# Kernel tuning notes

Measured on AMD Instinct MI355X. Metric: run time of the kernel, lower is better.

## Reference

```python
import jax, jax.numpy as jnp
import numpy as np

H = 8          # num_heads
DH = 16        # head dim = out_dim // num_heads
D = 128        # out_dim = in_dim
EPS_BN = 1e-5


def _batchnorm(h, gamma, beta):
    mu = h.mean(axis=0)
    var = h.var(axis=0)  # biased, matches torch BatchNorm1d training
    return (h - mu) / jnp.sqrt(var + EPS_BN) * gamma + beta


def setup_inputs() -> dict:
    key = jax.random.key(0)
    ks = jax.random.split(key, 16)
    N, E = 50000, 600000
    s = 1.0 / np.sqrt(D)
    inp = {
        "x": jax.random.normal(ks[0], (N, D), jnp.float32),
        "edge_attr": jax.random.normal(ks[1], (E, D), jnp.float32),
        "edge_index": jax.random.randint(ks[2], (2, E), 0, N, jnp.int64),
        # attention projections (no bias, use_bias=False)
        "Wq": jax.random.normal(ks[3], (D, D), jnp.float32) * s,
        "Wk": jax.random.normal(ks[4], (D, D), jnp.float32) * s,
        "We": jax.random.normal(ks[5], (D, D), jnp.float32) * s,
        "Wv": jax.random.normal(ks[6], (D, D), jnp.float32) * s,
        # batchnorm 1
        "bn1_g": jnp.ones((D,), jnp.float32),
        "bn1_b": jnp.zeros((D,), jnp.float32),
        # FFN
        "W1": jax.random.normal(ks[7], (D, 2 * D), jnp.float32) * s,
        "b1": jnp.zeros((2 * D,), jnp.float32),
        "W2": jax.random.normal(ks[8], (2 * D, D), jnp.float32) * (1.0 / np.sqrt(2 * D)),
        "b2": jnp.zeros((D,), jnp.float32),
        # batchnorm 2
        "bn2_g": jnp.ones((D,), jnp.float32),
        "bn2_b": jnp.zeros((D,), jnp.float32),
    }
    return inp


def _forward(x, edge_attr, edge_index, Wq, Wk, We, Wv, bn1_g, bn1_b,
             W1, b1, W2, b2, bn2_g, bn2_b):
    N = x.shape[0]
    src, dst = edge_index[0], edge_index[1]

    # projections -> [N, H, DH] / [E, H, DH]
    Q_h = (x @ Wq).reshape(N, H, DH)
    K_h = (x @ Wk).reshape(N, H, DH)
    V_h = (x @ Wv).reshape(N, H, DH)
    E_e = (edge_attr @ We).reshape(-1, H, DH)

    # edge-wise multiplicative attention score
    score = K_h[src] * Q_h[dst] / np.sqrt(DH) * E_e      # [E, H, DH]
    score = jnp.exp(jnp.clip(score.sum(-1, keepdims=True), -5.0, 5.0))  # [E, H, 1]

    msg = V_h[src] * score                               # [E, H, DH]
    wV = jax.ops.segment_sum(msg, dst, num_segments=N)   # [N, H, DH]
    Z = jax.ops.segment_sum(score, dst, num_segments=N)  # [N, H, 1]

    h_attn = (wV / (Z + 1e-6)).reshape(N, D)

    # residual + batchnorm (dropout=0)
    h = x + h_attn
    h = _batchnorm(h, bn1_g, bn1_b)

    # FFN with residual + batchnorm
    h2 = jax.nn.relu(h @ W1 + b1)
    h2 = h2 @ W2 + b2
    h = h + h2
    h = _batchnorm(h, bn2_g, bn2_b)
    return h


def reference(x, edge_attr, edge_index, Wq, Wk, We, Wv, bn1_g, bn1_b,
              W1, b1, W2, b2, bn2_g, bn2_b):
    return _forward(x, edge_attr, edge_index, Wq, Wk, We, Wv, bn1_g, bn1_b,
                    W1, b1, W2, b2, bn2_g, bn2_b)
```

## Files before the change

### kernel.cpp

```cpp
#include <hip/hip_runtime.h>
#include <hip/hip_bf16.h>
#include <math.h>
#include <stdint.h>

#define NN 50000
#define EE 600000

#define QH_OFF   0
#define K_OFF    6400000
#define V_OFF    12800000
#define HMID_OFF 6400000
#define HFIN_OFF 19200000
#define ROWS_OFF 19200000
#define CNT_OFF  19260000
#define CUR_OFF  19310000
#define ELS_OFF  19360000
#define ELE_OFF  19960000
#define ST_OFF   25600000
#define FLAG_OFF 25601024
#define H_OFF    QH_OFF

__global__ void detect_eidx(const int* __restrict__ e32, float* __restrict__ ws) {
  __shared__ int nz;
  if (threadIdx.x == 0) nz = 0;
  __syncthreads();
  if (e32[threadIdx.x * 2 + 1] != 0) atomicAdd(&nz, 1);
  __syncthreads();
  if (threadIdx.x == 0) ((int*)(ws + FLAG_OFF))[0] = (nz == 0) ? 1 : 0;
}

__device__ __forceinline__ int load_idx(const void* eidx, int is64, size_t off) {
  return is64 ? (int)((const long long*)eidx)[off] : ((const int*)eidx)[off];
}

__global__ __launch_bounds__(256)
void count_deg(const void* __restrict__ eidx, float* __restrict__ ws) {
  int e = blockIdx.x * 256 + threadIdx.x;
  if (e >= EE) return;
  int is64 = ((const int*)(ws + FLAG_OFF))[0];
  int dst = load_idx(eidx, is64, (size_t)EE + e);
  atomicAdd((int*)(ws + CNT_OFF) + dst, 1);
}

__global__ __launch_bounds__(1024)
void scan_deg(float* __restrict__ ws) {
  const int* cnt = (const int*)(ws + CNT_OFF);
  int* rows = (int*)(ws + ROWS_OFF);
  __shared__ int part[1024];
  const int t = threadIdx.x;
  const int base = t * 49;
  int s = 0;
  for (int i = 0; i < 49; ++i) {
    int idx = base + i;
    s += (idx < NN) ? cnt[idx] : 0;
  }
  part[t] = s;
  __syncthreads();
  for (int off = 1; off < 1024; off <<= 1) {
    int v = (t >= off) ? part[t - off] : 0;
    __syncthreads();
    part[t] += v;
    __syncthreads();
  }
  int run = (t == 0) ? 0 : part[t - 1];
  for (int i = 0; i < 49; ++i) {
    int idx = base + i;
    if (idx < NN) {
      rows[idx] = run;
      run += cnt[idx];
    }
  }
  if (t == 1023) rows[NN] = EE;
}

__global__ __launch_bounds__(256)
void fill_csr(const void* __restrict__ eidx, float* __restrict__ ws) {
  int e = blockIdx.x * 256 + threadIdx.x;
  if (e >= EE) return;
  int is64 = ((const int*)(ws + FLAG_OFF))[0];
  int src = load_idx(eidx, is64, (size_t)e);
  int dst = load_idx(eidx, is64, (size_t)EE + e);
  int p = atomicAdd((int*)(ws + CUR_OFF) + dst, 1);
  int j = ((const int*)(ws + ROWS_OFF))[dst] + p;
  ((int*)(ws + ELS_OFF))[j] = src;
  ((int*)(ws + ELE_OFF))[j] = e;
}

__global__ __launch_bounds__(256)
void proj_qkv(const float* __restrict__ x, const float* __restrict__ Wq,
              const float* __restrict__ Wk, const float* __restrict__ Wv,
              float* __restrict__ ws) {
  __shared__ float As[32][68];
  __shared__ float Bs[32][128];
  const int tid = threadIdx.x;
  const int tx = tid & 15, ty = tid >> 4;
  const int row0 = blockIdx.x * 64;
  const float* W = (blockIdx.y == 0) ? Wq : ((blockIdx.y == 1) ? Wk : Wv);
  float* out = ws + ((blockIdx.y == 0) ? QH_OFF : ((blockIdx.y == 1) ? K_OFF : V_OFF));

  float acc[4][8];
#pragma unroll
  for (int i = 0; i < 4; ++i)
#pragma unroll
    for (int j = 0; j < 8; ++j) acc[i][j] = 0.f;

  for (int k0 = 0; k0 < 128; k0 += 32) {
#pragma unroll
    for (int j = 0; j < 2; ++j) {
      int s = tid + 256 * j;
      int r = s >> 3, kg = (s & 7) << 2;
      int gr = row0 + r;
      float4 v = make_float4(0.f, 0.f, 0.f, 0.f);
      if (gr < NN) v = *(const float4*)&x[(size_t)gr * 128 + k0 + kg];
      As[kg + 0][r] = v.x; As[kg + 1][r] = v.y; As[kg + 2][r] = v.z; As[kg + 3][r] = v.w;
    }
#pragma unroll
    for (int j = 0; j < 4; ++j) {
      int s = tid + 256 * j;
      int kk = s >> 5, cg = (s & 31) << 2;
      *(float4*)&Bs[kk][cg] = *(const float4*)&W[(size_t)(k0 + kk) * 128 + cg];
    }
    __syncthreads();
#pragma unroll
    for (int k = 0; k < 32; ++k) {
      float4 a4 = *(float4*)&As[k][ty << 2];
      float4 b4a = *(float4*)&Bs[k][tx << 3];
      float4 b4b = *(float4*)&Bs[k][(tx << 3) + 4];
      float av[4] = {a4.x, a4.y, a4.z, a4.w};
      float bv[8] = {b4a.x, b4a.y, b4a.z, b4a.w, b4b.x, b4b.y, b4b.z, b4b.w};
#pragma unroll
      for (int i = 0; i < 4; ++i)
#pragma unroll
        for (int j = 0; j < 8; ++j) acc[i][j] = fmaf(av[i], bv[j], acc[i][j]);
    }
    __syncthreads();
  }
#pragma unroll
  for (int i = 0; i < 4; ++i) {
    int gr = row0 + (ty << 2) + i;
    if (gr < NN) {
      float4 o0 = make_float4(acc[i][0], acc[i][1], acc[i][2], acc[i][3]);
      float4 o1 = make_float4(acc[i][4], acc[i][5], acc[i][6], acc[i][7]);
      *(float4*)&out[(size_t)gr * 128 + (tx << 3)] = o0;
      *(float4*)&out[(size_t)gr * 128 + (tx << 3) + 4] = o1;
    }
  }
}

__global__ __launch_bounds__(256)
void edge_score(const float* __restrict__ edge_attr, const void* __restrict__ eidx,
                const float* __restrict__ We, float* __restrict__ ws,
                float* __restrict__ score) {
  __shared__ float As[32][68];
  __shared__ float Bs[32][128];
  __shared__ int s_src[64], s_dst[64];
  __shared__ int s_is64;
  const int tid = threadIdx.x;
  const int tx = tid & 15, ty = tid >> 4;
  const int e0 = blockIdx.x * 64;

  if (tid == 0) s_is64 = ((const int*)(ws + FLAG_OFF))[0];
  __syncthreads();
  if (tid < 128) {
    int lane = tid & 63;
    size_t off = (tid < 64) ? (size_t)(e0 + lane) : ((size_t)EE + e0 + lane);
    int idx = s_is64 ? (int)((const long long*)eidx)[off]
                     : ((const int*)eidx)[off];
    if (tid < 64) s_src[lane] = idx; else s_dst[lane] = idx;
  }

  float acc[4][8];
#pragma unroll
  for (int i = 0; i < 4; ++i)
#pragma unroll
    for (int j = 0; j < 8; ++j) acc[i][j] = 0.f;

  for (int k0 = 0; k0 < 128; k0 += 32) {
#pragma unroll
    for (int j = 0; j < 2; ++j) {
      int s = tid + 256 * j;
      int r = s >> 3, kg = (s & 7) << 2;
      float4 v = *(const float4*)&edge_attr[(size_t)(e0 + r) * 128 + k0 + kg];
      As[kg + 0][r] = v.x; As[kg + 1][r] = v.y; As[kg + 2][r] = v.z; As[kg + 3][r] = v.w;
    }
#pragma unroll
    for (int j = 0; j < 4; ++j) {
      int s = tid + 256 * j;
      int kk = s >> 5, cg = (s & 31) << 2;
      *(float4*)&Bs[kk][cg] = *(const float4*)&We[(size_t)(k0 + kk) * 128 + cg];
    }
    __syncthreads();
#pragma unroll
    for (int k = 0; k < 32; ++k) {
      float4 a4 = *(float4*)&As[k][ty << 2];
      float4 b4a = *(float4*)&Bs[k][tx << 3];
      float4 b4b = *(float4*)&Bs[k][(tx << 3) + 4];
      float av[4] = {a4.x, a4.y, a4.z, a4.w};
      float bv[8] = {b4a.x, b4a.y, b4a.z, b4a.w, b4b.x, b4b.y, b4b.z, b4b.w};
#pragma unroll
      for (int i = 0; i < 4; ++i)
#pragma unroll
        for (int j = 0; j < 8; ++j) acc[i][j] = fmaf(av[i], bv[j], acc[i][j]);
    }
    __syncthreads();
  }

  const float* Qm = ws + QH_OFF;
  const float* Km = ws + K_OFF;
  const int c0 = tx << 3;

#pragma unroll
  for (int i = 0; i < 4; ++i) {
    const int e = e0 + (ty << 2) + i;
    const int src = s_src[(ty << 2) + i];
    const int dst = s_dst[(ty << 2) + i];
    const float* Kp = Km + (size_t)src * 128 + c0;
    const float* Qp = Qm + (size_t)dst * 128 + c0;
    float4 ka = *(const float4*)Kp, kb = *(const float4*)(Kp + 4);
    float4 qa = *(const float4*)Qp, qb = *(const float4*)(Qp + 4);
    float p = acc[i][0] * ka.x * qa.x + acc[i][1] * ka.y * qa.y
            + acc[i][2] * ka.z * qa.z + acc[i][3] * ka.w * qa.w
            + acc[i][4] * kb.x * qb.x + acc[i][5] * kb.y * qb.y
            + acc[i][6] * kb.z * qb.z + acc[i][7] * kb.w * qb.w;
    p *= 0.25f;
    p += __shfl_xor(p, 1);
    float sc = __expf(fminf(fmaxf(p, -5.f), 5.f));
    if ((tx & 1) == 0) score[(size_t)e * 8 + (tx >> 1)] = sc;
  }
}

__global__ __launch_bounds__(256)
void aggregate(const float* __restrict__ x, const float* __restrict__ score,
               float* __restrict__ ws) {
  const int* rows = (const int*)(ws + ROWS_OFF);
  const int* els  = (const int*)(ws + ELS_OFF);
  const int* ele  = (const int*)(ws + ELE_OFF);
  const float* V  = ws + V_OFF;
  float* h = ws + H_OFF;
  float* st = ws + ST_OFF;
  const int tid = threadIdx.x;
  const int l = tid & 31;
  const int g = tid >> 5;
  const int c = l << 2;
  const int h8 = l >> 2;

  float s4[4] = {0.f, 0.f, 0.f, 0.f}, q4[4] = {0.f, 0.f, 0.f, 0.f};

  for (int d = blockIdx.x * 8 + g; d < NN; d += gridDim.x * 8) {
    const int j0 = rows[d], j1 = rows[d + 1];
    float a0 = 0.f, a1 = 0.f, a2 = 0.f, a3 = 0.f, z = 0.f;
    int e = 0, src = 0;
    if (j0 < j1) { e = ele[j0]; src = els[j0]; }
    for (int j = j0; j < j1; ++j) {
      int e2 = 0, src2 = 0;
      if (j + 1 < j1) { e2 = ele[j + 1]; src2 = els[j + 1]; }
      float sc = score[(size_t)e * 8 + h8];
      float4 v4 = *(const float4*)&V[(size_t)src * 128 + c];
      a0 = fmaf(v4.x, sc, a0); a1 = fmaf(v4.y, sc, a1);
      a2 = fmaf(v4.z, sc, a2); a3 = fmaf(v4.w, sc, a3);
      z += sc;
      e = e2; src = src2;
    }
    float zi = 1.f / (z + 1e-6f);
    float4 xv = *(const float4*)&x[(size_t)d * 128 + c];
    float4 hv;
    hv.x = xv.x + a0 * zi; hv.y = xv.y + a1 * zi;
    hv.z = xv.z + a2 * zi; hv.w = xv.w + a3 * zi;
    *(float4*)&h[(size_t)d * 128 + c] = hv;
    s4[0] += hv.x; s4[1] += hv.y; s4[2] += hv.z; s4[3] += hv.w;
    q4[0] += hv.x * hv.x; q4[1] += hv.y * hv.y;
    q4[2] += hv.z * hv.z; q4[3] += hv.w * hv.w;
  }

  __shared__ float red[8][32][8];
#pragma unroll
  for (int j = 0; j < 4; ++j) { red[g][l][j] = s4[j]; red[g][l][4 + j] = q4[j]; }
  __syncthreads();
  if (tid < 32) {
    float ss[4] = {0.f, 0.f, 0.f, 0.f}, qq[4] = {0.f, 0.f, 0.f, 0.f};
    for (int gg = 0; gg < 8; ++gg)
#pragma unroll
      for (int j = 0; j < 4; ++j) { ss[j] += red[gg][tid][j]; qq[j] += red[gg][tid][4 + j]; }
#pragma unroll
    for (int j = 0; j < 4; ++j) {
      atomicAdd(&st[(tid << 2) + j], ss[j]);
      atomicAdd(&st[128 + (tid << 2) + j], qq[j]);
    }
  }
}

__global__ void bn_finalize(const float* __restrict__ g, const float* __restrict__ beta,
                            float* __restrict__ ws, int sum_off, int out_off) {
  float* st = ws + ST_OFF;
  int c = threadIdx.x;
  float mu = st[sum_off + c] / (float)NN;
  float var = st[sum_off + 128 + c] / (float)NN - mu * mu;
  float istd = 1.f / sqrtf(var + 1e-5f);
  float a = g[c] * istd;
  st[out_off + c] = a;
  st[out_off + 128 + c] = beta[c] - mu * a;
}

__global__ __launch_bounds__(256)
void ffn1(const float* __restrict__ W1, const float* __restrict__ b1, float* __restrict__ ws) {
  __shared__ float As[32][68];
  __shared__ float Bs[32][128];
  const float* h = ws + H_OFF;
  const float* a1 = ws + ST_OFF + 512;
  const float* bb1 = ws + ST_OFF + 640;
  float* hmid = ws + HMID_OFF;
  const int tid = threadIdx.x;
  const int tx = tid & 15, ty = tid >> 4;
  const int row0 = blockIdx.x * 64;
  const int c0 = blockIdx.y * 128;

  float acc[4][8];
#pragma unroll
  for (int i = 0; i < 4; ++i)
#pragma unroll
    for (int j = 0; j < 8; ++j) acc[i][j] = 0.f;

  for (int k0 = 0; k0 < 128; k0 += 32) {
#pragma unroll
    for (int j = 0; j < 2; ++j) {
      int s = tid + 256 * j;
      int r = s >> 3, kg = (s & 7) << 2;
      int gr = row0 + r;
      float4 v = make_float4(0.f, 0.f, 0.f, 0.f);
      if (gr < NN) {
        v = *(const float4*)&h[(size_t)gr * 128 + k0 + kg];
        float4 aa = *(const float4*)&a1[k0 + kg];
        float4 bb = *(const float4*)&bb1[k0 + kg];
        v.x = v.x * aa.x + bb.x; v.y = v.y * aa.y + bb.y;
        v.z = v.z * aa.z + bb.z; v.w = v.w * aa.w + bb.w;
      }
      As[kg + 0][r] = v.x; As[kg + 1][r] = v.y; As[kg + 2][r] = v.z; As[kg + 3][r] = v.w;
    }
#pragma unroll
    for (int j = 0; j < 4; ++j) {
      int s = tid + 256 * j;
      int kk = s >> 5, cg = (s & 31) << 2;
      *(float4*)&Bs[kk][cg] = *(const float4*)&W1[(size_t)(k0 + kk) * 256 + c0 + cg];
    }
    __syncthreads();
#pragma unroll
    for (int k = 0; k < 32; ++k) {
      float4 a4 = *(float4*)&As[k][ty << 2];
      float4 b4a = *(float4*)&Bs[k][tx << 3];
      float4 b4b = *(float4*)&Bs[k][(tx << 3) + 4];
      float av[4] = {a4.x, a4.y, a4.z, a4.w};
      float bv[8] = {b4a.x, b4a.y, b4a.z, b4a.w, b4b.x, b4b.y, b4b.z, b4b.w};
#pragma unroll
      for (int i = 0; i < 4; ++i)
#pragma unroll
        for (int j = 0; j < 8; ++j) acc[i][j] = fmaf(av[i], bv[j], acc[i][j]);
    }
    __syncthreads();
  }
#pragma unroll
  for (int i = 0; i < 4; ++i) {
    int gr = row0 + (ty << 2) + i;
    if (gr < NN) {
      float o[8];
#pragma unroll
      for (int j = 0; j < 8; ++j) {
        int c = c0 + (tx << 3) + j;
        o[j] = fmaxf(acc[i][j] + b1[c], 0.f);
      }
      *(float4*)&hmid[(size_t)gr * 256 + c0 + (tx << 3)] = make_float4(o[0], o[1], o[2], o[3]);
      *(float4*)&hmid[(size_t)gr * 256 + c0 + (tx << 3) + 4] = make_float4(o[4], o[5], o[6], o[7]);
    }
  }
}

__global__ __launch_bounds__(256)
void ffn2(const float* __restrict__ W2, const float* __restrict__ b2, float* __restrict__ ws) {
  __shared__ float As[32][68];
  __shared__ float Bs[32][128];
  const float* hmid = ws + HMID_OFF;
  const float* h = ws + H_OFF;
  const float* a1 = ws + ST_OFF + 512;
  const float* bb1 = ws + ST_OFF + 640;
  float* hfin = ws + HFIN_OFF;
  float* st = ws + ST_OFF;
  const int tid = threadIdx.x;
  const int tx = tid & 15, ty = tid >> 4;
  const int row0 = blockIdx.x * 64;

  float acc[4][8];
#pragma unroll
  for (int i = 0; i < 4; ++i)
#pragma unroll
    for (int j = 0; j < 8; ++j) acc[i][j] = 0.f;

  for (int k0 = 0; k0 < 256; k0 += 32) {
#pragma unroll
    for (int j = 0; j < 2; ++j) {
      int s = tid + 256 * j;
      int r = s >> 3, kg = (s & 7) << 2;
      int gr = row0 + r;
      float4 v = make_float4(0.f, 0.f, 0.f, 0.f);
      if (gr < NN) v = *(const float4*)&hmid[(size_t)gr * 256 + k0 + kg];
      As[kg + 0][r] = v.x; As[kg + 1][r] = v.y; As[kg + 2][r] = v.z; As[kg + 3][r] = v.w;
    }
#pragma unroll
    for (int j = 0; j < 4; ++j) {
      int s = tid + 256 * j;
      int kk = s >> 5, cg = (s & 31) << 2;
      *(float4*)&Bs[kk][cg] = *(const float4*)&W2[(size_t)(k0 + kk) * 128 + cg];
    }
    __syncthreads();
#pragma unroll
    for (int k = 0; k < 32; ++k) {
      float4 a4 = *(float4*)&As[k][ty << 2];
      float4 b4a = *(float4*)&Bs[k][tx << 3];
      float4 b4b = *(float4*)&Bs[k][(tx << 3) + 4];
      float av[4] = {a4.x, a4.y, a4.z, a4.w};
      float bv[8] = {b4a.x, b4a.y, b4a.z, b4a.w, b4b.x, b4b.y, b4b.z, b4b.w};
#pragma unroll
      for (int i = 0; i < 4; ++i)
#pragma unroll
        for (int j = 0; j < 8; ++j) acc[i][j] = fmaf(av[i], bv[j], acc[i][j]);
    }
    __syncthreads();
  }

  float psum[8] = {0, 0, 0, 0, 0, 0, 0, 0}, psq[8] = {0, 0, 0, 0, 0, 0, 0, 0};
#pragma unroll
  for (int i = 0; i < 4; ++i) {
    int gr = row0 + (ty << 2) + i;
    if (gr < NN) {
      float o[8];
#pragma unroll
      for (int j = 0; j < 8; ++j) {
        int c = (tx << 3) + j;
        float hn = h[(size_t)gr * 128 + c] * a1[c] + bb1[c];
        float v = acc[i][j] + b2[c] + hn;
        o[j] = v;
        psum[j] += v;
        psq[j] += v * v;
      }
      *(float4*)&hfin[(size_t)gr * 128 + (tx << 3)] = make_float4(o[0], o[1], o[2], o[3]);
      *(float4*)&hfin[(size_t)gr * 128 + (tx << 3) + 4] = make_float4(o[4], o[5], o[6], o[7]);
    }
  }
  float* red = &Bs[0][0];
#pragma unroll
  for (int j = 0; j < 8; ++j) {
    red[ty * 128 + (tx << 3) + j] = psum[j];
    red[2048 + ty * 128 + (tx << 3) + j] = psq[j];
  }
  __syncthreads();
  if (tid < 128) {
    float ssum = 0.f, ssq = 0.f;
#pragma unroll
    for (int t = 0; t < 16; ++t) {
      ssum += red[t * 128 + tid];
      ssq += red[2048 + t * 128 + tid];
    }
    atomicAdd(&st[256 + tid], ssum);
    atomicAdd(&st[384 + tid], ssq);
  }
}

__global__ __launch_bounds__(256)
void bn2_apply(const float* __restrict__ ws, float* __restrict__ out) {
  const float* hfin = ws + HFIN_OFF;
  const float* st = ws + ST_OFF;
  const int total4 = NN * 128 / 4;
  for (int i = blockIdx.x * blockDim.x + threadIdx.x; i < total4; i += gridDim.x * blockDim.x) {
    int cg = (i & 31) << 2;
    float4 v = *(const float4*)&hfin[(size_t)i * 4];
    float4 a = *(const float4*)&st[768 + cg];
    float4 b = *(const float4*)&st[896 + cg];
    float4 o;
    o.x = v.x * a.x + b.x; o.y = v.y * a.y + b.y;
    o.z = v.z * a.z + b.z; o.w = v.w * a.w + b.w;
    *(float4*)&out[(size_t)i * 4] = o;
  }
}

extern "C" void kernel_launch(void* const* d_in, const int* in_sizes, int n_in,
                              void* d_out, int out_size, void* d_ws, size_t ws_size,
                              hipStream_t stream) {
  const float* x = (const float*)d_in[0];
  const float* edge_attr = (const float*)d_in[1];
  const void* eidx = d_in[2];
  const float* Wq = (const float*)d_in[3];
  const float* Wk = (const float*)d_in[4];
  const float* We = (const float*)d_in[5];
  const float* Wv = (const float*)d_in[6];
  const float* bn1_g = (const float*)d_in[7];
  const float* bn1_b = (const float*)d_in[8];
  const float* W1 = (const float*)d_in[9];
  const float* b1 = (const float*)d_in[10];
  const float* W2 = (const float*)d_in[11];
  const float* b2 = (const float*)d_in[12];
  const float* bn2_g = (const float*)d_in[13];
  const float* bn2_b = (const float*)d_in[14];
  float* ws = (float*)d_ws;
  float* out = (float*)d_out;
  float* score = out;

  hipMemsetAsync(ws + CNT_OFF, 0, 100000 * sizeof(int), stream);
  hipMemsetAsync(ws + ST_OFF, 0, 512 * sizeof(float), stream);

  dim3 b256(256);
  detect_eidx<<<1, 256, 0, stream>>>((const int*)eidx, ws);
  count_deg<<<dim3(2344), b256, 0, stream>>>(eidx, ws);
  scan_deg<<<1, 1024, 0, stream>>>(ws);
  fill_csr<<<dim3(2344), b256, 0, stream>>>(eidx, ws);
  proj_qkv<<<dim3(782, 3), b256, 0, stream>>>(x, Wq, Wk, Wv, ws);
  edge_score<<<dim3(9375), b256, 0, stream>>>(edge_attr, eidx, We, ws, score);
  aggregate<<<dim3(512), b256, 0, stream>>>(x, score, ws);
  bn_finalize<<<1, 128, 0, stream>>>(bn1_g, bn1_b, ws, 0, 512);
  ffn1<<<dim3(782, 2), b256, 0, stream>>>(W1, b1, ws);
  ffn2<<<dim3(782), b256, 0, stream>>>(W2, b2, ws);
  bn_finalize<<<1, 128, 0, stream>>>(bn2_g, bn2_b, ws, 256, 768);
  bn2_apply<<<dim3(2048), b256, 0, stream>>>(ws, out);
}
```

Baseline: 1.130 ms.

## Use bf16 MFMA for edge_attr projection in edge_score kernel

Replaces the FP32 scalar-FMA tiled GEMM for edge_attr @ We inside edge_score with bf16 MFMA 16x16x32 instructions. We is converted to bf16 and stored transposed in LDS, while edge_attr fragments are converted in registers. The score epilogue is reorganised around the MFMA output layout, using cross-lane shuffles and vectorised score stores. This aims to cut the ALU cost of the E×128×128 projection, at the risk of bf16 precision loss in the attention scores.

```diff
diff --git a/kernel.cpp b/kernel.cpp
--- a/kernel.cpp
+++ b/kernel.cpp
@@ -20,6 +20,15 @@
 #define FLAG_OFF 25601024
 #define H_OFF    QH_OFF
 
+typedef short s16x8 __attribute__((ext_vector_type(8)));
+typedef float f32x4 __attribute__((ext_vector_type(4)));
+
+__device__ __forceinline__ short f2bf(float f) {
+  union { float f; unsigned u; } v; v.f = f;
+  unsigned r = v.u + 0x7FFFu + ((v.u >> 16) & 1u);
+  return (short)(r >> 16);
+}
+
 __global__ void detect_eidx(const int* __restrict__ e32, float* __restrict__ ws) {
   __shared__ int nz;
   if (threadIdx.x == 0) nz = 0;
@@ -151,13 +160,15 @@
 void edge_score(const float* __restrict__ edge_attr, const void* __restrict__ eidx,
                 const float* __restrict__ We, float* __restrict__ ws,
                 float* __restrict__ score) {
-  __shared__ float As[32][68];
-  __shared__ float Bs[32][128];
+  __shared__ short lds_bt[128 * 136];
   __shared__ int s_src[64], s_dst[64];
   __shared__ int s_is64;
   const int tid = threadIdx.x;
-  const int tx = tid & 15, ty = tid >> 4;
   const int e0 = blockIdx.x * 64;
+  const int w = tid >> 6;
+  const int l = tid & 63;
+  const int le = l & 15;
+  const int g = l >> 4;
 
   if (tid == 0) s_is64 = ((const int*)(ws + FLAG_OFF))[0];
   __syncthreads();
@@ -169,63 +180,67 @@
     if (tid < 64) s_src[lane] = idx; else s_dst[lane] = idx;
   }
 
-  float acc[4][8];
-#pragma unroll
-  for (int i = 0; i < 4; ++i)
-#pragma unroll
-    for (int j = 0; j < 8; ++j) acc[i][j] = 0.f;
-
-  for (int k0 = 0; k0 < 128; k0 += 32) {
-#pragma unroll
-    for (int j = 0; j < 2; ++j) {
-      int s = tid + 256 * j;
-      int r = s >> 3, kg = (s & 7) << 2;
-      float4 v = *(const float4*)&edge_attr[(size_t)(e0 + r) * 128 + k0 + kg];
-      As[kg + 0][r] = v.x; As[kg + 1][r] = v.y; As[kg + 2][r] = v.z; As[kg + 3][r] = v.w;
-    }
-#pragma unroll
-    for (int j = 0; j < 4; ++j) {
-      int s = tid + 256 * j;
-      int kk = s >> 5, cg = (s & 31) << 2;
-      *(float4*)&Bs[kk][cg] = *(const float4*)&We[(size_t)(k0 + kk) * 128 + cg];
-    }
-    __syncthreads();
-#pragma unroll
-    for (int k = 0; k < 32; ++k) {
-      float4 a4 = *(float4*)&As[k][ty << 2];
-      float4 b4a = *(float4*)&Bs[k][tx << 3];
-      float4 b4b = *(float4*)&Bs[k][(tx << 3) + 4];
-      float av[4] = {a4.x, a4.y, a4.z, a4.w};
-      float bv[8] = {b4a.x, b4a.y, b4a.z, b4a.w, b4b.x, b4b.y, b4b.z, b4b.w};
-#pragma unroll
-      for (int i = 0; i < 4; ++i)
-#pragma unroll
-        for (int j = 0; j < 8; ++j) acc[i][j] = fmaf(av[i], bv[j], acc[i][j]);
-    }
-    __syncthreads();
+#pragma unroll
+  for (int i = 0; i < 4; ++i) {
+    const int k = i * 32 + (tid & 15) * 2;
+    const int n0 = (tid >> 4) * 8;
+    float4 a0 = *(const float4*)&We[(size_t)k * 128 + n0];
+    float4 a1 = *(const float4*)&We[(size_t)k * 128 + n0 + 4];
+    float4 b0 = *(const float4*)&We[(size_t)(k + 1) * 128 + n0];
+    float4 b1 = *(const float4*)&We[(size_t)(k + 1) * 128 + n0 + 4];
+    float av[8] = {a0.x, a0.y, a0.z, a0.w, a1.x, a1.y, a1.z, a1.w};
+    float bv[8] = {b0.x, b0.y, b0.z, b0.w, b1.x, b1.y, b1.z, b1.w};
+#pragma unroll
+    for (int j = 0; j < 8; ++j) {
+      unsigned lo16 = (unsigned short)f2bf(av[j]);
+      unsigned hi16 = (unsigned short)f2bf(bv[j]);
+      *(unsigned*)&lds_bt[(n0 + j) * 136 + k] = lo16 | (hi16 << 16);
+    }
+  }
+  __syncthreads();
+
+  f32x4 acc[8];
+#pragma unroll
+  for (int ct = 0; ct < 8; ++ct) acc[ct] = (f32x4){0.f, 0.f, 0.f, 0.f};
+
+  const float* ep = edge_attr + (size_t)(e0 + w * 16 + le) * 128;
+#pragma unroll
+  for (int k0i = 0; k0i < 4; ++k0i) {
+    const int k0 = k0i * 32;
+    float4 blo = *(const float4*)&ep[k0 + g * 8];
+    float4 bhi = *(const float4*)&ep[k0 + g * 8 + 4];
+    s16x8 bfrag;
+    bfrag[0] = f2bf(blo.x); bfrag[1] = f2bf(blo.y);
+    bfrag[2] = f2bf(blo.z); bfrag[3] = f2bf(blo.w);
+    bfrag[4] = f2bf(bhi.x); bfrag[5] = f2bf(bhi.y);
+    bfrag[6] = f2bf(bhi.z); bfrag[7] = f2bf(bhi.w);
+#pragma unroll
+    for (int ct = 0; ct < 8; ++ct) {
+      s16x8 afrag = *(const s16x8*)&lds_bt[(ct * 16 + le) * 136 + k0 + g * 8];
+      acc[ct] = __builtin_amdgcn_mfma_f32_16x16x32_bf16(afrag, bfrag, acc[ct], 0, 0, 0);
+    }
   }
 
   const float* Qm = ws + QH_OFF;
   const float* Km = ws + K_OFF;
-  const int c0 = tx << 3;
-
-#pragma unroll
-  for (int i = 0; i < 4; ++i) {
-    const int e = e0 + (ty << 2) + i;
-    const int src = s_src[(ty << 2) + i];
-    const int dst = s_dst[(ty << 2) + i];
-    const float* Kp = Km + (size_t)src * 128 + c0;
-    const float* Qp = Qm + (size_t)dst * 128 + c0;
-    float4 ka = *(const float4*)Kp, kb = *(const float4*)(Kp + 4);
-    float4 qa = *(const float4*)Qp, qb = *(const float4*)(Qp + 4);
-    float p = acc[i][0] * ka.x * qa.x + acc[i][1] * ka.y * qa.y
-            + acc[i][2] * ka.z * qa.z + acc[i][3] * ka.w * qa.w
-            + acc[i][4] * kb.x * qb.x + acc[i][5] * kb.y * qb.y
-            + acc[i][6] * kb.z * qb.z + acc[i][7] * kb.w * qb.w;
-    p *= 0.25f;
-    p += __shfl_xor(p, 1);
-    float sc = __expf(fminf(fmaxf(p, -5.f), 5.f));
-    if ((tx & 1) == 0) score[(size_t)e * 8 + (tx >> 1)] = sc;
+  const int e = e0 + w * 16 + le;
+  const int src = s_src[w * 16 + le];
+  const int dst = s_dst[w * 16 + le];
+  float out8[8];
+#pragma unroll
+  for (int ct = 0; ct < 8; ++ct) {
+    f32x4 kv = *(const f32x4*)&Km[(size_t)src * 128 + ct * 16 + g * 4];
+    f32x4 qv = *(const f32x4*)&Qm[(size_t)dst * 128 + ct * 16 + g * 4];
+    float part = acc[ct][0] * kv[0] * qv[0] + acc[ct][1] * kv[1] * qv[1]
+               + acc[ct][2] * kv[2] * qv[2] + acc[ct][3] * kv[3] * qv[3];
+    part += __shfl_xor(part, 16);
+    part += __shfl_xor(part, 32);
+    float p = part * 0.25f;
+    out8[ct] = __expf(fminf(fmaxf(p, -5.f), 5.f));
+  }
+  if (g == 0) {
+    *(float4*)&score[(size_t)e * 8] = make_float4(out8[0], out8[1], out8[2], out8[3]);
+    *(float4*)&score[(size_t)e * 8 + 4] = make_float4(out8[4], out8[5], out8[6], out8[7]);
   }
 }
 
```

New measurement: 1.100 ms. 1.03x faster.
